# Kernel tuning notes

Measured on AMD Instinct MI355X. Metric: run time of the kernel, lower is better.

Reference implementation:

```python
import jax, jax.numpy as jnp
import numpy as np


def setup_inputs() -> dict:
    key = jax.random.key(0)
    k1, k2, k3 = jax.random.split(key, 3)
    B, C = 8192, 10000
    inp = jax.random.normal(k1, (B, C), dtype=jnp.float32)
    distance_matrix = jax.random.uniform(k2, (C, C), dtype=jnp.float32)
    target = jax.random.randint(k3, (B,), 0, C, dtype=jnp.int64)
    return {"input": inp, "distance_matrix": distance_matrix, "target": target}


def reference(input, distance_matrix, target):
    B = input.shape[0]
    C = distance_matrix.shape[0]
    # vectorized replacement for the per-sample narrow+cat loop: row gather
    distance_vector = distance_matrix[target]  # [B, C]
    # NOTE: original uses log_softmax over dim=0 (batch dim) here — faithful.
    log_sm_batch = jax.nn.log_softmax(input, axis=0)  # [B, C]
    inclusive_reg = -0.5 * jnp.sum(distance_vector * log_sm_batch) / (C * B)
    # standard cross entropy (softmax over class dim, mean over batch)
    log_sm_cls = jax.nn.log_softmax(input, axis=1)  # [B, C]
    ce = -jnp.mean(jnp.take_along_axis(log_sm_cls, target[:, None], axis=1))
    return ce + inclusive_reg
```

## Files before the change

### kernel.cpp

```cpp
#include <hip/hip_runtime.h>

#define B_DIM 8192
#define C_DIM 10000
#define C4    2500
#define NT    10
#define TILE4 256
#define NCHUNK 128
#define ROWCHUNK (B_DIM / NCHUNK)
#define NCB   157

typedef float v4f __attribute__((ext_vector_type(4)));

__global__ __launch_bounds__(256) void fused_main(
    const v4f* __restrict__ x4, const v4f* __restrict__ dm4,
    const int* __restrict__ target,
    v4f* __restrict__ colExpPart, v4f* __restrict__ colDPart,
    float* __restrict__ rowPartExp, float* __restrict__ rowPartDx,
    float* __restrict__ xt) {
    const int tile  = blockIdx.x;
    const int chunk = blockIdx.y;
    const int tid   = threadIdx.x;
    const int lane  = tid & 63;
    const int wave  = tid >> 6;
    const int base4 = tile * TILE4;
    const int row0  = chunk * ROWCHUNK;

    __shared__ int s_t[ROWCHUNK];
    __shared__ v4f sE[TILE4];
    __shared__ v4f sD[TILE4];

    for (int r = tid; r < ROWCHUNK; r += 256) s_t[r] = target[row0 + r];
    __syncthreads();

    int  col4[4];
    bool valid[4];
    v4f accE[4], accD[4];
#pragma unroll
    for (int it = 0; it < 4; ++it) {
        col4[it]  = base4 + it * 64 + lane;
        valid[it] = col4[it] < C4;
        accE[it] = (v4f){0.f, 0.f, 0.f, 0.f};
        accD[it] = (v4f){0.f, 0.f, 0.f, 0.f};
    }

    for (int r = wave; r < ROWCHUNK; r += 4) {
        const int row = row0 + r;
        const int t   = s_t[r];
        const v4f* xrow = x4 + (size_t)row * C4;
        const v4f* drow = dm4 + (size_t)t * C4;
        const int tq = t >> 2, tl = t & 3;
        float rowE = 0.f, rowDx = 0.f;
#pragma unroll
        for (int it = 0; it < 4; ++it) {
            if (!valid[it]) continue;
            v4f xv = __builtin_nontemporal_load(&xrow[col4[it]]);
            v4f dv = drow[col4[it]];
            float ex = __expf(xv.x), ey = __expf(xv.y),
                  ez = __expf(xv.z), ew = __expf(xv.w);
            accE[it].x += ex; accE[it].y += ey; accE[it].z += ez; accE[it].w += ew;
            rowE += (ex + ey) + (ez + ew);
            accD[it].x += dv.x; accD[it].y += dv.y;
            accD[it].z += dv.z; accD[it].w += dv.w;
            rowDx += dv.x * xv.x + dv.y * xv.y + dv.z * xv.z + dv.w * xv.w;
            if (col4[it] == tq) {
                float v = (tl == 0) ? xv.x : (tl == 1) ? xv.y
                        : (tl == 2) ? xv.z : xv.w;
                xt[row] = v;
            }
        }
#pragma unroll
        for (int off = 32; off > 0; off >>= 1) {
            rowE  += __shfl_down(rowE, off, 64);
            rowDx += __shfl_down(rowDx, off, 64);
        }
        if (lane == 0) {
            rowPartExp[(size_t)tile * B_DIM + row] = rowE;
            rowPartDx [(size_t)tile * B_DIM + row] = rowDx;
        }
    }

    if (wave == 0) {
#pragma unroll
        for (int it = 0; it < 4; ++it) {
            sE[it * 64 + lane] = accE[it];
            sD[it * 64 + lane] = accD[it];
        }
    }
    __syncthreads();
    for (int w = 1; w < 4; ++w) {
        if (wave == w) {
#pragma unroll
            for (int it = 0; it < 4; ++it) {
                sE[it * 64 + lane] += accE[it];
                sD[it * 64 + lane] += accD[it];
            }
        }
        __syncthreads();
    }
    const int colg = base4 + tid;
    if (colg < C4) {
        colExpPart[(size_t)chunk * C4 + colg] = sE[tid];
        colDPart [(size_t)chunk * C4 + colg] = sD[tid];
    }
}

__global__ __launch_bounds__(256) void fin2_kernel(
    const v4f* __restrict__ colExpPart, const v4f* __restrict__ colDPart,
    const float* __restrict__ rowPartExp, const float* __restrict__ rowPartDx,
    const float* __restrict__ xt, double* __restrict__ partials) {
    const int b   = blockIdx.x;
    const int tid = threadIdx.x;
    __shared__ double sred[256];

    if (b < NCB) {
        const int cl   = tid & 15;
        const int q    = tid >> 4;
        const int col4 = b * 16 + cl;
        v4f se = {0.f, 0.f, 0.f, 0.f};
        v4f sd = {0.f, 0.f, 0.f, 0.f};
        if (col4 < C4) {
            for (int c = q; c < NCHUNK; c += 16) {
                se += __builtin_nontemporal_load(&colExpPart[(size_t)c * C4 + col4]);
                sd += __builtin_nontemporal_load(&colDPart [(size_t)c * C4 + col4]);
            }
        }
        __shared__ v4f lE[256], lD[256];
        lE[tid] = se; lD[tid] = sd;
        __syncthreads();
        for (int s = 8; s > 0; s >>= 1) {
            if (q < s) { lE[tid] += lE[tid + s * 16]; lD[tid] += lD[tid + s * 16]; }
            __syncthreads();
        }
        double mine = 0.0;
        if (q == 0 && col4 < C4) {
            v4f e = lE[tid];
            v4f d = lD[tid];
            mine = (double)d.x * (double)__logf(e.x)
                 + (double)d.y * (double)__logf(e.y)
                 + (double)d.z * (double)__logf(e.z)
                 + (double)d.w * (double)__logf(e.w);
        }
        sred[tid] = mine;
        __syncthreads();
        for (int s = 128; s > 0; s >>= 1) {
            if (tid < s) sred[tid] += sred[tid + s];
            __syncthreads();
        }
        if (tid == 0) partials[b] = sred[0];
    } else {
        const int s = b - NCB;
        const int i = s * 256 + tid;
        float re = 0.f, rdx = 0.f;
#pragma unroll
        for (int t = 0; t < NT; ++t) {
            re  += rowPartExp[(size_t)t * B_DIM + i];
            rdx += rowPartDx [(size_t)t * B_DIM + i];
        }
        double mine  = (double)(__logf(re) - xt[i]);
        double mine2 = (double)rdx;
        __shared__ double sred2[256];
        sred[tid] = mine; sred2[tid] = mine2;
        __syncthreads();
        for (int st = 128; st > 0; st >>= 1) {
            if (tid < st) { sred[tid] += sred[tid + st]; sred2[tid] += sred2[tid + st]; }
            __syncthreads();
        }
        if (tid == 0) { partials[NCB + s] = sred[0]; partials[NCB + 32 + s] = sred2[0]; }
    }
}

__global__ void out_kernel(const double* __restrict__ partials,
                           float* __restrict__ out) {
    const int tid = threadIdx.x;
    double t2 = 0.0, ce = 0.0, dx = 0.0;
    for (int i = tid; i < NCB; i += 64) t2 += partials[i];
    if (tid < 32) {
        ce = partials[NCB + tid];
        dx = partials[NCB + 32 + tid];
    }
#pragma unroll
    for (int off = 32; off > 0; off >>= 1) {
        t2 += __shfl_down(t2, off, 64);
        ce += __shfl_down(ce, off, 64);
        dx += __shfl_down(dx, off, 64);
    }
    if (tid == 0) {
        double ce_mean = ce / (double)B_DIM;
        double reg = -0.5 * (dx - t2) / ((double)C_DIM * (double)B_DIM);
        out[0] = (float)(ce_mean + reg);
    }
}

extern "C" void kernel_launch(void* const* d_in, const int* in_sizes, int n_in,
                              void* d_out, int out_size, void* d_ws, size_t ws_size,
                              hipStream_t stream) {
    const v4f* x4  = (const v4f*)d_in[0];
    const v4f* dm4 = (const v4f*)d_in[1];
    const int* target = (const int*)d_in[2];
    float* out = (float*)d_out;

    char* p = (char*)d_ws;
    auto alloc = [&](size_t bytes) {
        void* r = (void*)p;
        p += (bytes + 15) & ~(size_t)15;
        return r;
    };
    v4f*    colExpPart = (v4f*)alloc((size_t)NCHUNK * C4 * 16);
    v4f*    colDPart   = (v4f*)alloc((size_t)NCHUNK * C4 * 16);
    float*  rowPartExp = (float*)alloc((size_t)NT * B_DIM * 4);
    float*  rowPartDx  = (float*)alloc((size_t)NT * B_DIM * 4);
    float*  xt         = (float*)alloc((size_t)B_DIM * 4);
    double* partials   = (double*)alloc((NCB + 64) * 8);

    fused_main<<<dim3(NT, NCHUNK), 256, 0, stream>>>(
        x4, dm4, target, colExpPart, colDPart, rowPartExp, rowPartDx, xt);
    fin2_kernel<<<NCB + 32, 256, 0, stream>>>(
        colExpPart, colDPart, rowPartExp, rowPartDx, xt, partials);
    out_kernel<<<1, 64, 0, stream>>>(partials, out);
}
```

Measured before the change: 110.0 us.

## Merge three kernels into one persistent launch with atomic-counter handoff

Fuses the main reduction, epilogue, and final output kernels into a single launch. Epilogue blocks spin on a global atomic counter until all main blocks finish, and the last epilogue block (found via a second counter) computes the final scalar. This removes two kernel launch gaps but adds a memset launch and spinning blocks. The spinning blocks occupy CU slots while main blocks are still running, and the scheme relies on block scheduling order to avoid deadlock. The column-sum block reduction is also simplified to a 16-entry shared sum.

```diff
diff --git a/kernel.cpp b/kernel.cpp
--- a/kernel.cpp
+++ b/kernel.cpp
@@ -8,114 +8,135 @@
 #define NCHUNK 128
 #define ROWCHUNK (B_DIM / NCHUNK)
 #define NCB   157
+#define MAIN_BLOCKS (NT * NCHUNK)
+#define EPI_BLOCKS  (NCB + 32)
+#define SMEM_BYTES  10256
 
 typedef float v4f __attribute__((ext_vector_type(4)));
 
-__global__ __launch_bounds__(256) void fused_main(
+__global__ __launch_bounds__(256) void mega_kernel(
     const v4f* __restrict__ x4, const v4f* __restrict__ dm4,
     const int* __restrict__ target,
     v4f* __restrict__ colExpPart, v4f* __restrict__ colDPart,
     float* __restrict__ rowPartExp, float* __restrict__ rowPartDx,
-    float* __restrict__ xt) {
-    const int tile  = blockIdx.x;
-    const int chunk = blockIdx.y;
-    const int tid   = threadIdx.x;
-    const int lane  = tid & 63;
-    const int wave  = tid >> 6;
-    const int base4 = tile * TILE4;
-    const int row0  = chunk * ROWCHUNK;
-
-    __shared__ int s_t[ROWCHUNK];
-    __shared__ v4f sE[TILE4];
-    __shared__ v4f sD[TILE4];
-
-    for (int r = tid; r < ROWCHUNK; r += 256) s_t[r] = target[row0 + r];
-    __syncthreads();
-
-    int  col4[4];
-    bool valid[4];
-    v4f accE[4], accD[4];
-#pragma unroll
-    for (int it = 0; it < 4; ++it) {
-        col4[it]  = base4 + it * 64 + lane;
-        valid[it] = col4[it] < C4;
-        accE[it] = (v4f){0.f, 0.f, 0.f, 0.f};
-        accD[it] = (v4f){0.f, 0.f, 0.f, 0.f};
-    }
-
-    for (int r = wave; r < ROWCHUNK; r += 4) {
-        const int row = row0 + r;
-        const int t   = s_t[r];
-        const v4f* xrow = x4 + (size_t)row * C4;
-        const v4f* drow = dm4 + (size_t)t * C4;
-        const int tq = t >> 2, tl = t & 3;
-        float rowE = 0.f, rowDx = 0.f;
-#pragma unroll
-        for (int it = 0; it < 4; ++it) {
-            if (!valid[it]) continue;
-            v4f xv = __builtin_nontemporal_load(&xrow[col4[it]]);
-            v4f dv = drow[col4[it]];
-            float ex = __expf(xv.x), ey = __expf(xv.y),
-                  ez = __expf(xv.z), ew = __expf(xv.w);
-            accE[it].x += ex; accE[it].y += ey; accE[it].z += ez; accE[it].w += ew;
-            rowE += (ex + ey) + (ez + ew);
-            accD[it].x += dv.x; accD[it].y += dv.y;
-            accD[it].z += dv.z; accD[it].w += dv.w;
-            rowDx += dv.x * xv.x + dv.y * xv.y + dv.z * xv.z + dv.w * xv.w;
-            if (col4[it] == tq) {
-                float v = (tl == 0) ? xv.x : (tl == 1) ? xv.y
-                        : (tl == 2) ? xv.z : xv.w;
-                xt[row] = v;
-            }
-        }
-#pragma unroll
-        for (int off = 32; off > 0; off >>= 1) {
-            rowE  += __shfl_down(rowE, off, 64);
-            rowDx += __shfl_down(rowDx, off, 64);
-        }
-        if (lane == 0) {
-            rowPartExp[(size_t)tile * B_DIM + row] = rowE;
-            rowPartDx [(size_t)tile * B_DIM + row] = rowDx;
-        }
-    }
-
-    if (wave == 0) {
-#pragma unroll
-        for (int it = 0; it < 4; ++it) {
-            sE[it * 64 + lane] = accE[it];
-            sD[it * 64 + lane] = accD[it];
-        }
-    }
-    __syncthreads();
-    for (int w = 1; w < 4; ++w) {
-        if (wave == w) {
-#pragma unroll
-            for (int it = 0; it < 4; ++it) {
-                sE[it * 64 + lane] += accE[it];
-                sD[it * 64 + lane] += accD[it];
-            }
-        }
-        __syncthreads();
-    }
-    const int colg = base4 + tid;
-    if (colg < C4) {
-        colExpPart[(size_t)chunk * C4 + colg] = sE[tid];
-        colDPart [(size_t)chunk * C4 + colg] = sD[tid];
-    }
-}
-
-__global__ __launch_bounds__(256) void fin2_kernel(
-    const v4f* __restrict__ colExpPart, const v4f* __restrict__ colDPart,
-    const float* __restrict__ rowPartExp, const float* __restrict__ rowPartDx,
-    const float* __restrict__ xt, double* __restrict__ partials) {
+    float* __restrict__ xt, double* __restrict__ partials,
+    unsigned int* __restrict__ counters, float* __restrict__ out) {
+    __shared__ __align__(16) char smem[SMEM_BYTES];
     const int b   = blockIdx.x;
     const int tid = threadIdx.x;
-    __shared__ double sred[256];
-
-    if (b < NCB) {
+
+    if (b < MAIN_BLOCKS) {
+        const int tile  = b % NT;
+        const int chunk = b / NT;
+        const int lane  = tid & 63;
+        const int wave  = tid >> 6;
+        const int base4 = tile * TILE4;
+        const int row0  = chunk * ROWCHUNK;
+
+        int* s_t = (int*)smem;
+        v4f* sE  = (v4f*)(smem + 256);
+        v4f* sD  = (v4f*)(smem + 256 + 4096);
+
+        for (int r = tid; r < ROWCHUNK; r += 256) s_t[r] = target[row0 + r];
+        __syncthreads();
+
+        int  col4[4];
+        bool valid[4];
+        v4f accE[4], accD[4];
+#pragma unroll
+        for (int it = 0; it < 4; ++it) {
+            col4[it]  = base4 + it * 64 + lane;
+            valid[it] = col4[it] < C4;
+            accE[it] = (v4f){0.f, 0.f, 0.f, 0.f};
+            accD[it] = (v4f){0.f, 0.f, 0.f, 0.f};
+        }
+
+        for (int r = wave; r < ROWCHUNK; r += 4) {
+            const int row = row0 + r;
+            const int t   = s_t[r];
+            const v4f* xrow = x4 + (size_t)row * C4;
+            const v4f* drow = dm4 + (size_t)t * C4;
+            const int tq = t >> 2, tl = t & 3;
+            float rowE = 0.f, rowDx = 0.f;
+#pragma unroll
+            for (int it = 0; it < 4; ++it) {
+                if (!valid[it]) continue;
+                v4f xv = __builtin_nontemporal_load(&xrow[col4[it]]);
+                v4f dv = drow[col4[it]];
+                float ex = __expf(xv.x), ey = __expf(xv.y),
+                      ez = __expf(xv.z), ew = __expf(xv.w);
+                accE[it].x += ex; accE[it].y += ey;
+                accE[it].z += ez; accE[it].w += ew;
+                rowE += (ex + ey) + (ez + ew);
+                accD[it].x += dv.x; accD[it].y += dv.y;
+                accD[it].z += dv.z; accD[it].w += dv.w;
+                rowDx += dv.x * xv.x + dv.y * xv.y + dv.z * xv.z + dv.w * xv.w;
+                if (col4[it] == tq) {
+                    float v = (tl == 0) ? xv.x : (tl == 1) ? xv.y
+                            : (tl == 2) ? xv.z : xv.w;
+                    xt[row] = v;
+                }
+            }
+#pragma unroll
+            for (int off = 32; off > 0; off >>= 1) {
+                rowE  += __shfl_down(rowE, off, 64);
+                rowDx += __shfl_down(rowDx, off, 64);
+            }
+            if (lane == 0) {
+                rowPartExp[(size_t)tile * B_DIM + row] = rowE;
+                rowPartDx [(size_t)tile * B_DIM + row] = rowDx;
+            }
+        }
+
+        if (wave == 0) {
+#pragma unroll
+            for (int it = 0; it < 4; ++it) {
+                sE[it * 64 + lane] = accE[it];
+                sD[it * 64 + lane] = accD[it];
+            }
+        }
+        __syncthreads();
+        for (int w = 1; w < 4; ++w) {
+            if (wave == w) {
+#pragma unroll
+                for (int it = 0; it < 4; ++it) {
+                    sE[it * 64 + lane] += accE[it];
+                    sD[it * 64 + lane] += accD[it];
+                }
+            }
+            __syncthreads();
+        }
+        const int colg = base4 + tid;
+        if (colg < C4) {
+            colExpPart[(size_t)chunk * C4 + colg] = sE[tid];
+            colDPart [(size_t)chunk * C4 + colg] = sD[tid];
+        }
+        __syncthreads();
+        if (tid == 0) {
+            __hip_atomic_fetch_add(&counters[0], 1u, __ATOMIC_RELEASE,
+                                   __HIP_MEMORY_SCOPE_AGENT);
+        }
+        return;
+    }
+
+    if (tid == 0) {
+        while (__hip_atomic_load(&counters[0], __ATOMIC_RELAXED,
+                                 __HIP_MEMORY_SCOPE_AGENT) <
+               (unsigned)MAIN_BLOCKS)
+            __builtin_amdgcn_s_sleep(16);
+    }
+    __syncthreads();
+    __builtin_amdgcn_fence(__ATOMIC_ACQUIRE, "agent");
+
+    double* sred = (double*)smem;
+    if (b < MAIN_BLOCKS + NCB) {
+        const int eb   = b - MAIN_BLOCKS;
         const int cl   = tid & 15;
         const int q    = tid >> 4;
-        const int col4 = b * 16 + cl;
+        const int col4 = eb * 16 + cl;
+        v4f* lE = (v4f*)smem;
+        v4f* lD = (v4f*)(smem + 4096);
+        double* csred = (double*)(smem + 8192);
         v4f se = {0.f, 0.f, 0.f, 0.f};
         v4f sd = {0.f, 0.f, 0.f, 0.f};
         if (col4 < C4) {
@@ -124,7 +145,6 @@
                 sd += __builtin_nontemporal_load(&colDPart [(size_t)c * C4 + col4]);
             }
         }
-        __shared__ v4f lE[256], lD[256];
         lE[tid] = se; lD[tid] = sd;
         __syncthreads();
         for (int s = 8; s > 0; s >>= 1) {
@@ -140,26 +160,28 @@
                  + (double)d.z * (double)__logf(e.z)
                  + (double)d.w * (double)__logf(e.w);
         }
-        sred[tid] = mine;
-        __syncthreads();
-        for (int s = 128; s > 0; s >>= 1) {
-            if (tid < s) sred[tid] += sred[tid + s];
-            __syncthreads();
-        }
-        if (tid == 0) partials[b] = sred[0];
+        csred[tid >> 4] = 0.0;
+        __syncthreads();
+        if (q == 0) csred[cl] = mine;
+        __syncthreads();
+        if (tid == 0) {
+            double t2 = 0.0;
+#pragma unroll
+            for (int k = 0; k < 16; ++k) t2 += csred[k];
+            partials[eb] = t2;
+        }
     } else {
-        const int s = b - NCB;
+        const int s = b - MAIN_BLOCKS - NCB;
         const int i = s * 256 + tid;
+        double* sred2 = (double*)(smem + 2048);
         float re = 0.f, rdx = 0.f;
 #pragma unroll
         for (int t = 0; t < NT; ++t) {
             re  += rowPartExp[(size_t)t * B_DIM + i];
             rdx += rowPartDx [(size_t)t * B_DIM + i];
         }
-        double mine  = (double)(__logf(re) - xt[i]);
-        double mine2 = (double)rdx;
-        __shared__ double sred2[256];
-        sred[tid] = mine; sred2[tid] = mine2;
+        sred[tid]  = (double)(__logf(re) - xt[i]);
+        sred2[tid] = (double)rdx;
         __syncthreads();
         for (int st = 128; st > 0; st >>= 1) {
             if (tid < st) { sred[tid] += sred[tid + st]; sred2[tid] += sred2[tid + st]; }
@@ -167,27 +189,33 @@
         }
         if (tid == 0) { partials[NCB + s] = sred[0]; partials[NCB + 32 + s] = sred2[0]; }
     }
-}
-
-__global__ void out_kernel(const double* __restrict__ partials,
-                           float* __restrict__ out) {
-    const int tid = threadIdx.x;
-    double t2 = 0.0, ce = 0.0, dx = 0.0;
-    for (int i = tid; i < NCB; i += 64) t2 += partials[i];
-    if (tid < 32) {
-        ce = partials[NCB + tid];
-        dx = partials[NCB + 32 + tid];
-    }
-#pragma unroll
-    for (int off = 32; off > 0; off >>= 1) {
-        t2 += __shfl_down(t2, off, 64);
-        ce += __shfl_down(ce, off, 64);
-        dx += __shfl_down(dx, off, 64);
-    }
+
+    int* s_win = (int*)(smem + 10240);
+    __syncthreads();
     if (tid == 0) {
-        double ce_mean = ce / (double)B_DIM;
-        double reg = -0.5 * (dx - t2) / ((double)C_DIM * (double)B_DIM);
-        out[0] = (float)(ce_mean + reg);
+        unsigned old = __hip_atomic_fetch_add(&counters[1], 1u, __ATOMIC_ACQ_REL,
+                                              __HIP_MEMORY_SCOPE_AGENT);
+        *s_win = (old == (unsigned)(EPI_BLOCKS - 1));
+    }
+    __syncthreads();
+    if (*s_win && tid < 64) {
+        double t2 = 0.0, ce = 0.0, dx = 0.0;
+        for (int i = tid; i < NCB; i += 64) t2 += partials[i];
+        if (tid < 32) {
+            ce = partials[NCB + tid];
+            dx = partials[NCB + 32 + tid];
+        }
+#pragma unroll
+        for (int off = 32; off > 0; off >>= 1) {
+            t2 += __shfl_down(t2, off, 64);
+            ce += __shfl_down(ce, off, 64);
+            dx += __shfl_down(dx, off, 64);
+        }
+        if (tid == 0) {
+            double ce_mean = ce / (double)B_DIM;
+            double reg = -0.5 * (dx - t2) / ((double)C_DIM * (double)B_DIM);
+            out[0] = (float)(ce_mean + reg);
+        }
     }
 }
 
@@ -211,10 +239,11 @@
     float*  rowPartDx  = (float*)alloc((size_t)NT * B_DIM * 4);
     float*  xt         = (float*)alloc((size_t)B_DIM * 4);
     double* partials   = (double*)alloc((NCB + 64) * 8);
-
-    fused_main<<<dim3(NT, NCHUNK), 256, 0, stream>>>(
-        x4, dm4, target, colExpPart, colDPart, rowPartExp, rowPartDx, xt);
-    fin2_kernel<<<NCB + 32, 256, 0, stream>>>(
-        colExpPart, colDPart, rowPartExp, rowPartDx, xt, partials);
-    out_kernel<<<1, 64, 0, stream>>>(partials, out);
+    unsigned int* counters = (unsigned int*)alloc(2 * sizeof(unsigned int));
+
+    hipMemsetAsync(counters, 0, 2 * sizeof(unsigned int), stream);
+
+    mega_kernel<<<MAIN_BLOCKS + EPI_BLOCKS, 256, 0, stream>>>(
+        x4, dm4, target, colExpPart, colDPart, rowPartExp, rowPartDx, xt,
+        partials, counters, out);
 }
```

Result: slower. 214.3 us (+94.8%).

## Sort batch rows by target to reuse gathered distance-matrix rows

Applied to the files above, without the earlier changes.

Adds a single-block bitonic sort in shared memory that builds a permutation of batch rows ordered by target class. The main kernel then walks rows in that order, keeping each wave's rows contiguous, and reloads the distance-matrix row only when the target changes. The aim is to cut redundant distance-matrix gather traffic when targets repeat, and to improve cache locality. The cost is an extra serialized sort kernel with many barriers, plus scattered writes to the row-indexed outputs.

```diff
diff --git a/kernel.cpp b/kernel.cpp
--- a/kernel.cpp
+++ b/kernel.cpp
@@ -7,13 +7,38 @@
 #define TILE4 256
 #define NCHUNK 128
 #define ROWCHUNK (B_DIM / NCHUNK)
+#define WROWS (ROWCHUNK / 4)
 #define NCB   157
 
 typedef float v4f __attribute__((ext_vector_type(4)));
+
+__global__ __launch_bounds__(1024) void sort_kernel(
+    const int* __restrict__ target, unsigned* __restrict__ perm) {
+    __shared__ unsigned key[B_DIM];
+    const int tid = threadIdx.x;
+    for (int i = tid; i < B_DIM; i += 1024)
+        key[i] = ((unsigned)target[i] << 13) | (unsigned)i;
+    __syncthreads();
+    for (int k = 2; k <= B_DIM; k <<= 1) {
+        for (int j = k >> 1; j > 0; j >>= 1) {
+            for (int i = tid; i < B_DIM; i += 1024) {
+                const int ixj = i ^ j;
+                if (ixj > i) {
+                    const unsigned a = key[i], b = key[ixj];
+                    const bool asc = ((i & k) == 0);
+                    if ((a > b) == asc) { key[i] = b; key[ixj] = a; }
+                }
+            }
+            __syncthreads();
+        }
+    }
+    for (int i = tid; i < B_DIM; i += 1024)
+        perm[i] = key[i] & (B_DIM - 1);
+}
 
 __global__ __launch_bounds__(256) void fused_main(
     const v4f* __restrict__ x4, const v4f* __restrict__ dm4,
-    const int* __restrict__ target,
+    const int* __restrict__ target, const unsigned* __restrict__ perm,
     v4f* __restrict__ colExpPart, v4f* __restrict__ colDPart,
     float* __restrict__ rowPartExp, float* __restrict__ rowPartDx,
     float* __restrict__ xt) {
@@ -25,47 +50,61 @@
     const int base4 = tile * TILE4;
     const int row0  = chunk * ROWCHUNK;
 
+    __shared__ int s_sr[ROWCHUNK];
     __shared__ int s_t[ROWCHUNK];
     __shared__ v4f sE[TILE4];
     __shared__ v4f sD[TILE4];
 
-    for (int r = tid; r < ROWCHUNK; r += 256) s_t[r] = target[row0 + r];
+    for (int r = tid; r < ROWCHUNK; r += 256) {
+        const int sr = (int)perm[row0 + r];
+        s_sr[r] = sr;
+        s_t[r]  = target[sr];
+    }
     __syncthreads();
 
     int  col4[4];
     bool valid[4];
-    v4f accE[4], accD[4];
+    v4f accE[4], accD[4], dv[4];
 #pragma unroll
     for (int it = 0; it < 4; ++it) {
         col4[it]  = base4 + it * 64 + lane;
         valid[it] = col4[it] < C4;
         accE[it] = (v4f){0.f, 0.f, 0.f, 0.f};
         accD[it] = (v4f){0.f, 0.f, 0.f, 0.f};
-    }
-
-    for (int r = wave; r < ROWCHUNK; r += 4) {
-        const int row = row0 + r;
-        const int t   = s_t[r];
-        const v4f* xrow = x4 + (size_t)row * C4;
-        const v4f* drow = dm4 + (size_t)t * C4;
+        dv[it]   = (v4f){0.f, 0.f, 0.f, 0.f};
+    }
+
+    int prev_t = -1;
+    for (int rr = 0; rr < WROWS; ++rr) {
+        const int r    = wave * WROWS + rr;
+        const int srow = s_sr[r];
+        const int t    = s_t[r];
+        const v4f* xrow = x4 + (size_t)srow * C4;
+        if (t != prev_t) {
+            const v4f* drow = dm4 + (size_t)t * C4;
+#pragma unroll
+            for (int it = 0; it < 4; ++it)
+                if (valid[it]) dv[it] = drow[col4[it]];
+            prev_t = t;
+        }
         const int tq = t >> 2, tl = t & 3;
         float rowE = 0.f, rowDx = 0.f;
 #pragma unroll
         for (int it = 0; it < 4; ++it) {
             if (!valid[it]) continue;
             v4f xv = __builtin_nontemporal_load(&xrow[col4[it]]);
-            v4f dv = drow[col4[it]];
             float ex = __expf(xv.x), ey = __expf(xv.y),
                   ez = __expf(xv.z), ew = __expf(xv.w);
-            accE[it].x += ex; accE[it].y += ey; accE[it].z += ez; accE[it].w += ew;
+            accE[it].x += ex; accE[it].y += ey;
+            accE[it].z += ez; accE[it].w += ew;
             rowE += (ex + ey) + (ez + ew);
-            accD[it].x += dv.x; accD[it].y += dv.y;
-            accD[it].z += dv.z; accD[it].w += dv.w;
-            rowDx += dv.x * xv.x + dv.y * xv.y + dv.z * xv.z + dv.w * xv.w;
+            accD[it] += dv[it];
+            rowDx += dv[it].x * xv.x + dv[it].y * xv.y
+                   + dv[it].z * xv.z + dv[it].w * xv.w;
             if (col4[it] == tq) {
                 float v = (tl == 0) ? xv.x : (tl == 1) ? xv.y
                         : (tl == 2) ? xv.z : xv.w;
-                xt[row] = v;
+                xt[srow] = v;
             }
         }
 #pragma unroll
@@ -74,8 +113,8 @@
             rowDx += __shfl_down(rowDx, off, 64);
         }
         if (lane == 0) {
-            rowPartExp[(size_t)tile * B_DIM + row] = rowE;
-            rowPartDx [(size_t)tile * B_DIM + row] = rowDx;
+            rowPartExp[(size_t)tile * B_DIM + srow] = rowE;
+            rowPartDx [(size_t)tile * B_DIM + srow] = rowDx;
         }
     }
 
@@ -211,9 +250,11 @@
     float*  rowPartDx  = (float*)alloc((size_t)NT * B_DIM * 4);
     float*  xt         = (float*)alloc((size_t)B_DIM * 4);
     double* partials   = (double*)alloc((NCB + 64) * 8);
-
+    unsigned* perm     = (unsigned*)alloc((size_t)B_DIM * 4);
+
+    sort_kernel<<<1, 1024, 0, stream>>>(target, perm);
     fused_main<<<dim3(NT, NCHUNK), 256, 0, stream>>>(
-        x4, dm4, target, colExpPart, colDPart, rowPartExp, rowPartDx, xt);
+        x4, dm4, target, perm, colExpPart, colDPart, rowPartExp, rowPartDx, xt);
     fin2_kernel<<<NCB + 32, 256, 0, stream>>>(
         colExpPart, colDPart, rowPartExp, rowPartDx, xt, partials);
     out_kernel<<<1, 64, 0, stream>>>(partials, out);
```

Result: slower. 209.4 us (+90.4%).
